# Kernel optimization log

Hardware: AMD Instinct MI355X
Metric: run time of the kernel (lower is better)

## Reference

```python
import jax, jax.numpy as jnp
import numpy as np

B, T, D = 2, 2048, 2048
N, K, H = 16, 4, 128  # query heads, kv heads, head dim
G = N // K            # GQA groups
MIN_TS, MAX_TS = 1.0, 10000.0


def rope(x, positions):
    # x: [B, S, heads, H], positions: [B, S] int
    half = H // 2
    fraction = 2.0 * jnp.arange(half, dtype=jnp.float32) / H
    timescale = MIN_TS * (MAX_TS / MIN_TS) ** fraction            # [half]
    sinusoid = positions.astype(jnp.float32)[:, :, None, None] / timescale  # [B,S,1,half]
    sin, cos = jnp.sin(sinusoid), jnp.cos(sinusoid)
    x1, x2 = x[..., :half], x[..., half:]
    return jnp.concatenate([x1 * cos - x2 * sin, x2 * cos + x1 * sin], axis=-1)


def setup_inputs() -> dict:
    key = jax.random.key(0)
    ks = jax.random.split(key, 6)
    pos = jnp.tile(jnp.arange(T, dtype=jnp.int32)[None, :], (B, 1))
    return {
        "Xq": jax.random.normal(ks[0], (B, T, D), jnp.float32),
        "Xkv": jax.random.normal(ks[1], (B, T, D), jnp.float32),
        "q_positions": pos,
        "kv_positions": pos,
        "Wq": jax.random.normal(ks[2], (D, N, H), jnp.float32) * 0.02,
        "Wk": jax.random.normal(ks[3], (D, K, H), jnp.float32) * 0.02,
        "Wv": jax.random.normal(ks[4], (D, K, H), jnp.float32) * 0.02,
        "Wo": jax.random.normal(ks[5], (N, H, D), jnp.float32) * 0.02,
    }


def reference(Xq, Xkv, q_positions, kv_positions, Wq, Wk, Wv, Wo):
    # QKV projections (tensordot over embed dim), fp32
    q = jnp.einsum("btd,dnh->btnh", Xq, Wq)          # [B,T,N,H]
    k = jnp.einsum("bsd,dkh->bskh", Xkv, Wk)         # [B,S,K,H]
    v = jnp.einsum("bsd,dkh->bskh", Xkv, Wv)
    # inline RoPE on q and k
    q = rope(q, q_positions)
    k = rope(k, kv_positions)
    # GQA: group query heads over kv heads -> [B,K,G,T,H]
    qg = q.transpose(0, 2, 1, 3).reshape(B, K, G, T, H)
    kt = k.transpose(0, 2, 1, 3)                      # [B,K,S,H]
    vt = v.transpose(0, 2, 1, 3)
    scale = 1.0 / jnp.sqrt(jnp.float32(H))
    scores = jnp.einsum("bkgth,bksh->bkgts", qg, kt) * scale
    # causal mask (self-attn, no explicit mask, T>1)
    causal = jnp.tril(jnp.ones((T, T), dtype=bool))
    scores = jnp.where(causal[None, None, None], scores, jnp.finfo(scores.dtype).min)
    probs = jax.nn.softmax(scores, axis=-1)
    attn = jnp.einsum("bkgts,bksh->bkgth", probs, vt)  # [B,K,G,T,H]
    attn = attn.reshape(B, N, T, H).transpose(0, 2, 1, 3)  # [B,T,N,H]
    out = jnp.einsum("btnh,nhd->btd", attn, Wo)
    return out
```

## Files before the change

### kernel.cpp

```cpp
#include <hip/hip_runtime.h>
#include <hip/hip_bf16.h>
#include <cstdint>
#include <cstddef>

#define Bdim 2
#define Tdim 2048
#define Ddim 2048
#define NHq  16
#define NKV  4
#define HD   128
#define SCALE 0.08838834764831845f
#define QPRESCALE (0.08838834764831845f * 1.4426950408889634f)
#define NEG_INF (-3.0e38f)
#define DEFER_THR 11.5f

typedef unsigned short u16;
typedef unsigned int   u32;
typedef __bf16 bf16x8 __attribute__((ext_vector_type(8)));
typedef float  f32x4  __attribute__((ext_vector_type(4)));

__device__ __forceinline__ u16 f2bf(float f) {
    unsigned int u = __float_as_uint(f);
    u += 0x7FFFu + ((u >> 16) & 1u);
    return (u16)(u >> 16);
}
__device__ __forceinline__ u16 f2bfn(float f) {
    __bf16 h = (__bf16)f;
    return __builtin_bit_cast(u16, h);
}
__device__ __forceinline__ float bf2f(u16 s) {
    return __uint_as_float(((unsigned int)s) << 16);
}

#if __has_builtin(__builtin_amdgcn_permlane16_swap) && __has_builtin(__builtin_amdgcn_permlane32_swap)
#define HAVE_PERMLANE_SWAP 1
#endif

__device__ __forceinline__ float quad_reduce_max(float v) {
#ifdef HAVE_PERMLANE_SWAP
    auto r = __builtin_amdgcn_permlane16_swap(__float_as_uint(v), __float_as_uint(v), false, false);
    float m = fmaxf(__uint_as_float(r[0]), __uint_as_float(r[1]));
    auto r2 = __builtin_amdgcn_permlane32_swap(__float_as_uint(m), __float_as_uint(m), false, false);
    return fmaxf(__uint_as_float(r2[0]), __uint_as_float(r2[1]));
#else
    v = fmaxf(v, __shfl_xor(v, 16));
    return fmaxf(v, __shfl_xor(v, 32));
#endif
}
__device__ __forceinline__ float quad_reduce_sum(float v) {
#ifdef HAVE_PERMLANE_SWAP
    auto r = __builtin_amdgcn_permlane16_swap(__float_as_uint(v), __float_as_uint(v), false, false);
    float s = __uint_as_float(r[0]) + __uint_as_float(r[1]);
    auto r2 = __builtin_amdgcn_permlane32_swap(__float_as_uint(s), __float_as_uint(s), false, false);
    return __uint_as_float(r2[0]) + __uint_as_float(r2[1]);
#else
    v += __shfl_xor(v, 16);
    return v + __shfl_xor(v, 32);
#endif
}

__device__ __forceinline__ float tree_max16(const float (&s)[16]) {
    float a0 = fmaxf(s[0], s[1]),  a1 = fmaxf(s[2], s[3]);
    float a2 = fmaxf(s[4], s[5]),  a3 = fmaxf(s[6], s[7]);
    float a4 = fmaxf(s[8], s[9]),  a5 = fmaxf(s[10], s[11]);
    float a6 = fmaxf(s[12], s[13]), a7 = fmaxf(s[14], s[15]);
    float b0 = fmaxf(a0, a1), b1 = fmaxf(a2, a3);
    float b2 = fmaxf(a4, a5), b3 = fmaxf(a6, a7);
    return fmaxf(fmaxf(b0, b1), fmaxf(b2, b3));
}
__device__ __forceinline__ float tree_sum16(const float (&s)[16]) {
    float a0 = s[0] + s[1],  a1 = s[2] + s[3];
    float a2 = s[4] + s[5],  a3 = s[6] + s[7];
    float a4 = s[8] + s[9],  a5 = s[10] + s[11];
    float a6 = s[12] + s[13], a7 = s[14] + s[15];
    float b0 = a0 + a1, b1 = a2 + a3, b2 = a4 + a5, b3 = a6 + a7;
    return (b0 + b1) + (b2 + b3);
}

typedef __attribute__((address_space(1))) const u32 gbl_u32;
typedef __attribute__((address_space(3))) u32 lds_u32;
__device__ __forceinline__ void gload16(const void* g, void* l) {
    __builtin_amdgcn_global_load_lds((gbl_u32*)(uintptr_t)g, (lds_u32*)(uintptr_t)l, 16, 0, 0);
}

#define VM8 asm volatile("s_waitcnt vmcnt(8)" ::: "memory")
#define VM4 asm volatile("s_waitcnt vmcnt(4)" ::: "memory")
#define VM0 asm volatile("s_waitcnt vmcnt(0)" ::: "memory")
#define VMNONE ((void)0)
#define BARRIER do { asm volatile("" ::: "memory"); __builtin_amdgcn_s_barrier(); asm volatile("" ::: "memory"); } while (0)

__global__ __launch_bounds__(256) void prep_all(const float* __restrict__ Xq,
                                                const float* __restrict__ Xkv,
                                                const float* __restrict__ Wq,
                                                const float* __restrict__ Wk,
                                                const float* __restrict__ Wv,
                                                const float* __restrict__ Wo,
                                                u16* __restrict__ xq_bf,
                                                u16* __restrict__ xkv_bf,
                                                u16* __restrict__ wq_t,
                                                u16* __restrict__ wk_t,
                                                u16* __restrict__ wv_t,
                                                u16* __restrict__ wo_t)
{
    __shared__ u16 t[64][72];
    const int tid = threadIdx.x;
    int bid = blockIdx.x;

    if (bid < 8192) {
        const size_t NE = (size_t)4096 * 2048 / 8;
        size_t idx = (size_t)bid * 256 + tid;
        const float* src; u16* dst; size_t off;
        if (idx < NE) { src = Xq;  dst = xq_bf;  off = idx * 8; }
        else          { src = Xkv; dst = xkv_bf; off = (idx - NE) * 8; }
        float4 a = *(const float4*)&src[off];
        float4 b = *(const float4*)&src[off + 4];
        ushort4 r0, r1;
        r0.x = f2bf(a.x); r0.y = f2bf(a.y); r0.z = f2bf(a.z); r0.w = f2bf(a.w);
        r1.x = f2bf(b.x); r1.y = f2bf(b.y); r1.z = f2bf(b.z); r1.w = f2bf(b.w);
        *(ushort4*)&dst[off] = r0;
        *(ushort4*)&dst[off + 4] = r1;
        return;
    }
    bid -= 8192;
    const float* src; u16* dst; int C, gx;
    const int R = 2048;
    if (bid < 1024)      { src = Wq; dst = wq_t; C = 2048; gx = 32; }
    else if (bid < 1280) { src = Wk; dst = wk_t; C = 512;  gx = 8;  bid -= 1024; }
    else if (bid < 1536) { src = Wv; dst = wv_t; C = 512;  gx = 8;  bid -= 1280; }
    else                 { src = Wo; dst = wo_t; C = 2048; gx = 32; bid -= 1536; }

    const int r0 = (bid / gx) * 64, c0 = (bid % gx) * 64;
    const int tr = tid >> 4, tc4 = (tid & 15) * 4;
#pragma unroll
    for (int p = 0; p < 4; p++) {
        int r = p * 16 + tr;
        float4 v = *(const float4*)&src[(size_t)(r0 + r) * C + c0 + tc4];
        t[tc4 + 0][r] = f2bf(v.x);
        t[tc4 + 1][r] = f2bf(v.y);
        t[tc4 + 2][r] = f2bf(v.z);
        t[tc4 + 3][r] = f2bf(v.w);
    }
    __syncthreads();
#pragma unroll
    for (int p = 0; p < 4; p++) {
        int cc = p * 16 + tr;
        ushort4 w = *(const ushort4*)&t[cc][tc4];
        *(ushort4*)&dst[(size_t)(c0 + cc) * R + r0 + tc4] = w;
    }
}

__global__ __launch_bounds__(256) void rope_k(u16* __restrict__ k,
                                              const int* __restrict__ kvpos)
{
    int idx = blockIdx.x * 256 + threadIdx.x;
    int rn = idx >> 4;
    int h4 = (idx & 15) * 4;
    int pos = kvpos[rn >> 2];
    u16* base = k + (size_t)rn * HD;
    ushort4 a = *(const ushort4*)&base[h4];
    ushort4 bvec = *(const ushort4*)&base[h4 + 64];
    u16 av[4] = {a.x, a.y, a.z, a.w};
    u16 bv[4] = {bvec.x, bvec.y, bvec.z, bvec.w};
#pragma unroll
    for (int j = 0; j < 4; j++) {
        float inv_ts = expf(-(float)(h4 + j) * 0.14391156831f);
        float ang = (float)pos * inv_ts;
        float s, c;
        sincosf(ang, &s, &c);
        float x1 = bf2f(av[j]), x2 = bf2f(bv[j]);
        av[j] = f2bf(x1 * c - x2 * s);
        bv[j] = f2bf(x2 * c + x1 * s);
    }
    ushort4 ra, rb;
    ra.x = av[0]; ra.y = av[1]; ra.z = av[2]; ra.w = av[3];
    rb.x = bv[0]; rb.y = bv[1]; rb.z = bv[2]; rb.w = bv[3];
    *(ushort4*)&base[h4] = ra;
    *(ushort4*)&base[h4 + 64] = rb;
}

#define GPH(c, ks, mh, STAGE, VMW) do {                                        \
    bf16x8 Af[4];                                                              \
    _Pragma("unroll")                                                          \
    for (int mf = 0; mf < 4; mf++)                                             \
        Af[mf] = *(const bf16x8*)&Ab[c][ks][(arow + (mh) * 64 + mf * 16) * 32 + cxs]; \
    if ((mh) == 0) {                                                           \
        _Pragma("unroll")                                                      \
        for (int nf = 0; nf < 4; nf++)                                         \
            Bf[nf] = *(const bf16x8*)&Bb[c][ks][(brow + nf * 16) * 32 + cxs];  \
    }                                                                          \
    STAGE;                                                                     \
    BARRIER;                                                                   \
    asm volatile("s_waitcnt lgkmcnt(0)" ::: "memory");                         \
    __builtin_amdgcn_s_setprio(1);                                             \
    _Pragma("unroll")                                                          \
    for (int mf = 0; mf < 4; mf++)                                             \
        _Pragma("unroll")                                                      \
        for (int nf = 0; nf < 4; nf++)                                         \
            acc[(mh) * 4 + mf][nf] = __builtin_amdgcn_mfma_f32_16x16x32_bf16(  \
                Af[mf], Bf[nf], acc[(mh) * 4 + mf][nf], 0, 0, 0);              \
    __builtin_amdgcn_s_setprio(0);                                             \
    VMW;                                                                       \
    BARRIER;                                                                   \
} while (0)

__device__ __forceinline__ void gemm8_mainloop(const u16* __restrict__ A,
                                               const u16* __restrict__ Bt,
                                               int m0, int n0,
                                               u16 (&Ab)[2][2][256 * 32],
                                               u16 (&Bb)[2][2][256 * 32],
                                               f32x4 (&acc)[8][4])
{
    const int tid = threadIdx.x;
    const int wv = tid >> 6, lane = tid & 63;
    const int l15 = lane & 15, quad = lane >> 4;
    const int wr = wv >> 2, wc = wv & 3;

#pragma unroll
    for (int mf = 0; mf < 8; mf++)
#pragma unroll
        for (int nf = 0; nf < 4; nf++) acc[mf][nf] = (f32x4){0.f, 0.f, 0.f, 0.f};

    auto stageA = [&](int kt, int kh, int c) {
#pragma unroll
        for (int j = 0; j < 2; j++) {
            int q = j * 512 + tid;
            int r = q >> 2;
            int c4 = (q & 3) ^ (r & 3);
            gload16(A + (size_t)(m0 + r) * 2048 + kt * 64 + kh * 32 + c4 * 8,
                    &Ab[c][kh][q * 8]);
        }
    };
    auto stageB = [&](int kt, int kh, int c) {
#pragma unroll
        for (int j = 0; j < 2; j++) {
            int q = j * 512 + tid;
            int r = q >> 2;
            int c4 = (q & 3) ^ (r & 3);
            gload16(Bt + (size_t)(n0 + r) * 2048 + kt * 64 + kh * 32 + c4 * 8,
                    &Bb[c][kh][q * 8]);
        }
    };

    const int arow = wr * 128 + l15;
    const int brow = wc * 64 + l15;
    const int cxs  = (quad ^ (l15 & 3)) * 8;

    stageA(0, 0, 0); stageB(0, 0, 0);
    stageA(0, 1, 0); stageB(0, 1, 0);
    stageA(1, 0, 1); stageB(1, 0, 1);
    VM8;
    BARRIER;

    bf16x8 Bf[4];
    for (int it = 0; it < 15; it++) {
        const int t0 = 2 * it, t1 = 2 * it + 1;
        GPH(0, 0, 0, { stageA(t1, 1, 1); },     VMNONE);
        GPH(0, 0, 1, { stageB(t1, 1, 1); },     VM8);
        GPH(0, 1, 0, { stageA(t0 + 2, 0, 0); }, VMNONE);
        GPH(0, 1, 1, { stageB(t0 + 2, 0, 0); }, VM8);
        GPH(1, 0, 0, { stageA(t0 + 2, 1, 0); }, VMNONE);
        GPH(1, 0, 1, { stageB(t0 + 2, 1, 0); }, VM8);
        GPH(1, 1, 0, { stageA(t1 + 2, 0, 1); }, VMNONE);
        GPH(1, 1, 1, { stageB(t1 + 2, 0, 1); }, VM8);
    }
    GPH(0, 0, 0, { stageA(31, 1, 1); }, VMNONE);
    GPH(0, 0, 1, { stageB(31, 1, 1); }, VM8);
    GPH(0, 1, 0, VMNONE, VMNONE);
    GPH(0, 1, 1, VMNONE, VM4);
    GPH(1, 0, 0, VMNONE, VMNONE);
    GPH(1, 0, 1, VMNONE, VM0);
    GPH(1, 1, 0, VMNONE, VMNONE);
    GPH(1, 1, 1, VMNONE, VMNONE);
}

__global__ __launch_bounds__(512, 2) void qkv_gemm8(const u16* __restrict__ Xq,
                                                    const u16* __restrict__ Xkv,
                                                    const u16* __restrict__ Wqt,
                                                    const u16* __restrict__ Wkt,
                                                    const u16* __restrict__ Wvt,
                                                    u16* __restrict__ qraw,
                                                    u16* __restrict__ kraw,
                                                    u16* __restrict__ vt)
{
    __shared__ __align__(16) u16 Ab[2][2][256 * 32];
    __shared__ __align__(16) u16 Bb[2][2][256 * 32];
    f32x4 acc[8][4];

    const int bid0 = (int)blockIdx.x + 12 * (int)blockIdx.y;
    const int swz  = (bid0 & 7) * 24 + (bid0 >> 3);
    const int cx   = swz % 12;
    const int m0   = (swz / 12) * 256;

    const u16 *A, *Bt; int nb;
    if (cx < 8)       { A = Xq;  Bt = Wqt; nb = cx * 256; }
    else if (cx < 10) { A = Xkv; Bt = Wkt; nb = (cx - 8) * 256; }
    else              { A = Xkv; Bt = Wvt; nb = (cx - 10) * 256; }

    gemm8_mainloop(A, Bt, m0, nb, Ab, Bb, acc);

    const int tid = threadIdx.x;
    const int wv = tid >> 6, lane = tid & 63;
    const int l15 = lane & 15, quad = lane >> 4;
    const int wr = wv >> 2, wc = wv & 3;
    const int row0 = m0 + wr * 128;

    if (cx < 10) {
        u16* out; int ldw;
        if (cx < 8) { out = qraw; ldw = 2048; }
        else        { out = kraw; ldw = 512; }
#pragma unroll
        for (int mf = 0; mf < 8; mf++)
#pragma unroll
            for (int nf = 0; nf < 4; nf++) {
                int col = nb + wc * 64 + nf * 16 + l15;
                int r = row0 + mf * 16 + quad * 4;
#pragma unroll
                for (int reg = 0; reg < 4; reg++)
                    out[(size_t)(r + reg) * ldw + col] = f2bf(acc[mf][nf][reg]);
            }
    } else {
        const int b = m0 >> 11;
#pragma unroll
        for (int mf = 0; mf < 8; mf++)
#pragma unroll
            for (int nf = 0; nf < 4; nf++) {
                int col = nb + wc * 64 + nf * 16 + l15;
                int tloc = ((row0 & 2047) + mf * 16 + quad * 4);
                ushort4 w4;
                w4.x = f2bf(acc[mf][nf][0]);
                w4.y = f2bf(acc[mf][nf][1]);
                w4.z = f2bf(acc[mf][nf][2]);
                w4.w = f2bf(acc[mf][nf][3]);
                *(ushort4*)&vt[((size_t)(b * 512 + col)) * 2048 + tloc] = w4;
            }
    }
}

__global__ __launch_bounds__(512, 2) void oproj_gemm8(const u16* __restrict__ attnb,
                                                      const u16* __restrict__ Wot,
                                                      float* __restrict__ out)
{
    __shared__ __align__(16) u16 Ab[2][2][256 * 32];
    __shared__ __align__(16) u16 Bb[2][2][256 * 32];
    f32x4 acc[8][4];

    const int bid0 = (int)blockIdx.x + 8 * (int)blockIdx.y;
    const int swz  = (bid0 & 7) * 16 + (bid0 >> 3);
    const int n0   = (swz % 8) * 256;
    const int m0   = (swz / 8) * 256;

    gemm8_mainloop(attnb, Wot, m0, n0, Ab, Bb, acc);

    const int tid = threadIdx.x;
    const int wv = tid >> 6, lane = tid & 63;
    const int l15 = lane & 15, quad = lane >> 4;
    const int wr = wv >> 2, wc = wv & 3;
    const int row0 = m0 + wr * 128;
#pragma unroll
    for (int mf = 0; mf < 8; mf++)
#pragma unroll
        for (int nf = 0; nf < 4; nf++) {
            int col = n0 + wc * 64 + nf * 16 + l15;
            int r = row0 + mf * 16 + quad * 4;
#pragma unroll
            for (int reg = 0; reg < 4; reg++)
                out[(size_t)(r + reg) * 2048 + col] = acc[mf][nf][reg];
        }
}

__global__ __launch_bounds__(512, 4) void flash_attn_v6(const u16* __restrict__ qh,
                                                        const u16* __restrict__ kh,
                                                        const u16* __restrict__ vtg,
                                                        const int* __restrict__ qpos,
                                                        u16* __restrict__ attnb)
{
    __shared__ __align__(16) u16 Ks[2][64 * 128];
    __shared__ __align__(16) u16 Vt[2][128 * 64];
    __shared__ __align__(16) u16 Ps[128 * 64];

    const int yy = blockIdx.y;
    const int qt = (yy < 8) ? (15 - yy) : (yy - 8);
    const int bh = blockIdx.x;
    const int b = bh >> 4, n = bh & 15, kvh = n >> 2;
    const int q0 = qt * 128;
    const int tid = threadIdx.x;
    const int wv = tid >> 6, lane = tid & 63;
    const int l15 = lane & 15, quad = lane >> 4;

    const size_t kbase = (size_t)(b * Tdim) * 512 + kvh * 128;
    const size_t vbase = ((size_t)(b * 512 + kvh * 128)) * 2048;
    const int nT = 2 * qt + 2;

    auto stage = [&](int t, int buf) {
        const int s0s = t * 64;
#pragma unroll
        for (int c = 0; c < 2; c++) {
            int j = c * 512 + tid;
            int s = j >> 4;
            int c8 = (j & 15) ^ (s & 7);
            gload16(kh + kbase + (size_t)(s0s + s) * 512 + c8 * 8,
                    &Ks[buf][(c * 512 + wv * 64) * 8]);
            int h = j >> 3;
            int sb = (j & 7) ^ (h & 7);
            gload16(vtg + vbase + (size_t)h * 2048 + s0s + sb * 8,
                    &Vt[buf][(c * 512 + wv * 64) * 8]);
        }
    };

    stage(0, 0);

    bf16x8 qfrag[4];
    {
        const size_t qbase = ((size_t)(b * Tdim + q0 + wv * 16)) * 2048 + n * 128;
        float qv[4][8];
#pragma unroll
        for (int kt = 0; kt < 4; kt++) {
            bf16x8 raw = *(const bf16x8*)(qh + qbase + (size_t)l15 * 2048
                                           + kt * 32 + quad * 8);
#pragma unroll
            for (int j = 0; j < 8; j++) qv[kt][j] = (float)raw[j];
        }
        const int pos = qpos[b * Tdim + q0 + wv * 16 + l15];
#pragma unroll
        for (int kt = 0; kt < 2; kt++)
#pragma unroll
            for (int j = 0; j < 8; j++) {
                int h = kt * 32 + quad * 8 + j;
                float inv_ts = expf(-(float)h * 0.14391156831f);
                float s, c;
                sincosf((float)pos * inv_ts, &s, &c);
                s *= QPRESCALE; c *= QPRESCALE;
                float x1 = qv[kt][j], x2 = qv[kt + 2][j];
                qv[kt][j]     = x1 * c - x2 * s;
                qv[kt + 2][j] = x2 * c + x1 * s;
            }
#pragma unroll
        for (int kt = 0; kt < 4; kt++) {
            bf16x8 f;
#pragma unroll
            for (int j = 0; j < 8; j++) f[j] = (__bf16)qv[kt][j];
            qfrag[kt] = f;
        }
    }

    f32x4 Oacc[8];
#pragma unroll
    for (int ht = 0; ht < 8; ht++) Oacc[ht] = (f32x4){0.f, 0.f, 0.f, 0.f};
    float mrow = NEG_INF;
    float lrow = 0.f;

    __syncthreads();

    int cur = 0;
    for (int t = 0; t < nT; t++) {
        const int s0 = t * 64;

        if (t + 1 < nT) stage(t + 1, cur ^ 1);

        f32x4 S[4];
#pragma unroll
        for (int nt = 0; nt < 4; nt++) S[nt] = (f32x4){0.f, 0.f, 0.f, 0.f};
#pragma unroll
        for (int kt = 0; kt < 4; kt++) {
            bf16x8 kf[4];
#pragma unroll
            for (int nt = 0; nt < 4; nt++) {
                int s = nt * 16 + l15;
                int cb = (kt * 4 + quad) ^ (s & 7);
                kf[nt] = *(const bf16x8*)&Ks[cur][s * 128 + cb * 8];
            }
#pragma unroll
            for (int nt = 0; nt < 4; nt++)
                S[nt] = __builtin_amdgcn_mfma_f32_16x16x32_bf16(kf[nt], qfrag[kt], S[nt], 0, 0, 0);
        }

        const bool domask = (t >= nT - 2);
        const int m_l = wv * 16 + l15;
        const int mg = q0 + m_l;
        float sv[16];
#pragma unroll
        for (int nt = 0; nt < 4; nt++)
#pragma unroll
            for (int r = 0; r < 4; r++) {
                float vv = S[nt][r];
                if (domask) {
                    int sg = s0 + nt * 16 + quad * 4 + r;
                    if (sg > mg) vv = NEG_INF;
                }
                sv[nt * 4 + r] = vv;
            }
        float mx = quad_reduce_max(tree_max16(sv));
        const bool skip = __all(mx <= mrow + DEFER_THR);
        const float mNew = skip ? mrow : fmaxf(mrow, mx);
#pragma unroll
        for (int i = 0; i < 16; i++)
            sv[i] = __builtin_amdgcn_exp2f(sv[i] - mNew);
#pragma unroll
        for (int nt = 0; nt < 4; nt++) {
            int sb = nt * 2 + (quad >> 1);
            int cb = sb ^ (m_l & 7);
            ushort4 pw;
            pw.x = f2bfn(sv[nt * 4 + 0]);
            pw.y = f2bfn(sv[nt * 4 + 1]);
            pw.z = f2bfn(sv[nt * 4 + 2]);
            pw.w = f2bfn(sv[nt * 4 + 3]);
            *(ushort4*)&Ps[m_l * 64 + cb * 8 + (quad & 1) * 4] = pw;
        }
        {
            float ps = quad_reduce_sum(tree_sum16(sv));
            if (skip) {
                lrow += ps;
            } else {
                float alpha = __builtin_amdgcn_exp2f(mrow - mNew);
                mrow = mNew;
                lrow = lrow * alpha + ps;
                float a0 = __shfl(alpha, quad * 4 + 0);
                float a1 = __shfl(alpha, quad * 4 + 1);
                float a2 = __shfl(alpha, quad * 4 + 2);
                float a3 = __shfl(alpha, quad * 4 + 3);
#pragma unroll
                for (int ht = 0; ht < 8; ht++) {
                    Oacc[ht][0] *= a0;
                    Oacc[ht][1] *= a1;
                    Oacc[ht][2] *= a2;
                    Oacc[ht][3] *= a3;
                }
            }
        }

#pragma unroll
        for (int k2 = 0; k2 < 2; k2++) {
            int cbp = (k2 * 4 + quad) ^ (m_l & 7);
            bf16x8 pf = *(const bf16x8*)&Ps[m_l * 64 + cbp * 8];
#pragma unroll
            for (int ht = 0; ht < 8; ht++) {
                int h = ht * 16 + l15;
                int cb = (k2 * 4 + quad) ^ (h & 7);
                bf16x8 vf = *(const bf16x8*)&Vt[cur][h * 64 + cb * 8];
                Oacc[ht] = __builtin_amdgcn_mfma_f32_16x16x32_bf16(pf, vf, Oacc[ht], 0, 0, 0);
            }
        }

        __syncthreads();
        cur ^= 1;
    }

    {
        f32x4 inv;
#pragma unroll
        for (int r = 0; r < 4; r++)
            inv[r] = 1.0f / __shfl(lrow, quad * 4 + r);
        int mg0 = q0 + wv * 16 + quad * 4;
        u16* dst0 = attnb + ((size_t)(b * Tdim + mg0)) * 2048 + n * 128 + l15;
#pragma unroll
        for (int ht = 0; ht < 8; ht++) {
#pragma unroll
            for (int r = 0; r < 4; r++)
                dst0[(size_t)r * 2048 + ht * 16] = f2bfn(Oacc[ht][r] * inv[r]);
        }
    }
}

extern "C" void kernel_launch(void* const* d_in, const int* in_sizes, int n_in,
                              void* d_out, int out_size, void* d_ws, size_t ws_size,
                              hipStream_t stream) {
    const float* Xq    = (const float*)d_in[0];
    const float* Xkv   = (const float*)d_in[1];
    const int*   qpos  = (const int*)d_in[2];
    const int*   kvpos = (const int*)d_in[3];
    const float* Wq    = (const float*)d_in[4];
    const float* Wk    = (const float*)d_in[5];
    const float* Wv    = (const float*)d_in[6];
    const float* Wo    = (const float*)d_in[7];
    float* out = (float*)d_out;

    char* w = (char*)d_ws;
    u16* xq_bf = (u16*)(w);
    u16* xkv_bf= (u16*)(w + (16u << 20));
    u16* qraw  = (u16*)(w + (32u << 20));
    u16* kraw  = (u16*)(w + (48u << 20));
    u16* vt    = (u16*)(w + (52u << 20));
    u16* wq_t  = (u16*)(w + (56u << 20));
    u16* wk_t  = (u16*)(w + (64u << 20));
    u16* wv_t  = (u16*)(w + (66u << 20));
    u16* wo_t  = (u16*)(w + (68u << 20));
    u16* attnb = (u16*)(w);

    prep_all<<<10752, 256, 0, stream>>>(Xq, Xkv, Wq, Wk, Wv, Wo,
                                        xq_bf, xkv_bf, wq_t, wk_t, wv_t, wo_t);
    qkv_gemm8<<<dim3(12, 16), 512, 0, stream>>>(xq_bf, xkv_bf, wq_t, wk_t, wv_t,
                                                qraw, kraw, vt);
    rope_k<<<1024, 256, 0, stream>>>(kraw, kvpos);
    flash_attn_v6<<<dim3(32, 16), 512, 0, stream>>>(qraw, kraw, vt, qpos, attnb);
    oproj_gemm8<<<dim3(8, 16), 512, 0, stream>>>(attnb, wo_t, out);
}
```

Baseline: 349.0 us.

## Narrow o-proj GEMM tiles to 256x128 and use hardware sincos for RoPE

```diff
diff --git a/kernel.cpp b/kernel.cpp
--- a/kernel.cpp
+++ b/kernel.cpp
@@ -13,6 +13,8 @@
 #define QPRESCALE (0.08838834764831845f * 1.4426950408889634f)
 #define NEG_INF (-3.0e38f)
 #define DEFER_THR 11.5f
+#define ROPE_L2 0.20762051f
+#define INV_2PI 0.15915494f
 
 typedef unsigned short u16;
 typedef unsigned int   u32;
@@ -30,6 +32,12 @@
 }
 __device__ __forceinline__ float bf2f(u16 s) {
     return __uint_as_float(((unsigned int)s) << 16);
+}
+
+__device__ __forceinline__ void hw_sincos_rev(float rev, float* s, float* c) {
+    rev -= floorf(rev);
+    *s = __builtin_amdgcn_sinf(rev);
+    *c = __builtin_amdgcn_cosf(rev);
 }
 
 #if __has_builtin(__builtin_amdgcn_permlane16_swap) && __has_builtin(__builtin_amdgcn_permlane32_swap)
@@ -84,7 +92,9 @@
 }
 
 #define VM8 asm volatile("s_waitcnt vmcnt(8)" ::: "memory")
+#define VM6 asm volatile("s_waitcnt vmcnt(6)" ::: "memory")
 #define VM4 asm volatile("s_waitcnt vmcnt(4)" ::: "memory")
+#define VM3 asm volatile("s_waitcnt vmcnt(3)" ::: "memory")
 #define VM0 asm volatile("s_waitcnt vmcnt(0)" ::: "memory")
 #define VMNONE ((void)0)
 #define BARRIER do { asm volatile("" ::: "memory"); __builtin_amdgcn_s_barrier(); asm volatile("" ::: "memory"); } while (0)
@@ -163,10 +173,9 @@
     u16 bv[4] = {bvec.x, bvec.y, bvec.z, bvec.w};
 #pragma unroll
     for (int j = 0; j < 4; j++) {
-        float inv_ts = expf(-(float)(h4 + j) * 0.14391156831f);
-        float ang = (float)pos * inv_ts;
+        float rscale = __builtin_amdgcn_exp2f((float)(h4 + j) * -ROPE_L2) * INV_2PI;
         float s, c;
-        sincosf(ang, &s, &c);
+        hw_sincos_rev((float)pos * rscale, &s, &c);
         float x1 = bf2f(av[j]), x2 = bf2f(bv[j]);
         av[j] = f2bf(x1 * c - x2 * s);
         bv[j] = f2bf(x2 * c + x1 * s);
@@ -336,20 +345,112 @@
     }
 }
 
-__global__ __launch_bounds__(512, 2) void oproj_gemm8(const u16* __restrict__ attnb,
-                                                      const u16* __restrict__ Wot,
-                                                      float* __restrict__ out)
+#define GPHN(c, ks, mh, STAGE, VMW) do {                                       \
+    bf16x8 Af[4];                                                              \
+    _Pragma("unroll")                                                          \
+    for (int mf = 0; mf < 4; mf++)                                             \
+        Af[mf] = *(const bf16x8*)&Ab[c][ks][(arow + (mh) * 64 + mf * 16) * 32 + cxs]; \
+    if ((mh) == 0) {                                                           \
+        _Pragma("unroll")                                                      \
+        for (int nf = 0; nf < 2; nf++)                                         \
+            Bf[nf] = *(const bf16x8*)&Bb[c][ks][(brow + nf * 16) * 32 + cxs];  \
+    }                                                                          \
+    STAGE;                                                                     \
+    BARRIER;                                                                   \
+    asm volatile("s_waitcnt lgkmcnt(0)" ::: "memory");                         \
+    __builtin_amdgcn_s_setprio(1);                                             \
+    _Pragma("unroll")                                                          \
+    for (int mf = 0; mf < 4; mf++)                                             \
+        _Pragma("unroll")                                                      \
+        for (int nf = 0; nf < 2; nf++)                                         \
+            acc[(mh) * 4 + mf][nf] = __builtin_amdgcn_mfma_f32_16x16x32_bf16(  \
+                Af[mf], Bf[nf], acc[(mh) * 4 + mf][nf], 0, 0, 0);              \
+    __builtin_amdgcn_s_setprio(0);                                             \
+    VMW;                                                                       \
+    BARRIER;                                                                   \
+} while (0)
+
+__device__ __forceinline__ void gemm8n_mainloop(const u16* __restrict__ A,
+                                                const u16* __restrict__ Bt,
+                                                int m0, int n0,
+                                                u16 (&Ab)[2][2][256 * 32],
+                                                u16 (&Bb)[2][2][128 * 32],
+                                                f32x4 (&acc)[8][2])
+{
+    const int tid = threadIdx.x;
+    const int wv = tid >> 6, lane = tid & 63;
+    const int l15 = lane & 15, quad = lane >> 4;
+    const int wr = wv >> 2, wc = wv & 3;
+
+#pragma unroll
+    for (int mf = 0; mf < 8; mf++)
+#pragma unroll
+        for (int nf = 0; nf < 2; nf++) acc[mf][nf] = (f32x4){0.f, 0.f, 0.f, 0.f};
+
+    auto stageA = [&](int kt, int kh, int c) {
+#pragma unroll
+        for (int j = 0; j < 2; j++) {
+            int q = j * 512 + tid;
+            int r = q >> 2;
+            int c4 = (q & 3) ^ (r & 3);
+            gload16(A + (size_t)(m0 + r) * 2048 + kt * 64 + kh * 32 + c4 * 8,
+                    &Ab[c][kh][q * 8]);
+        }
+    };
+    auto stageB = [&](int kt, int kh, int c) {
+        int q = tid;
+        int r = q >> 2;
+        int c4 = (q & 3) ^ (r & 3);
+        gload16(Bt + (size_t)(n0 + r) * 2048 + kt * 64 + kh * 32 + c4 * 8,
+                &Bb[c][kh][q * 8]);
+    };
+
+    const int arow = wr * 128 + l15;
+    const int brow = wc * 32 + l15;
+    const int cxs  = (quad ^ (l15 & 3)) * 8;
+
+    stageA(0, 0, 0); stageB(0, 0, 0);
+    stageA(0, 1, 0); stageB(0, 1, 0);
+    stageA(1, 0, 1); stageB(1, 0, 1);
+    VM6;
+    BARRIER;
+
+    bf16x8 Bf[2];
+    for (int it = 0; it < 15; it++) {
+        const int t0 = 2 * it, t1 = 2 * it + 1;
+        GPHN(0, 0, 0, { stageA(t1, 1, 1); },     VMNONE);
+        GPHN(0, 0, 1, { stageB(t1, 1, 1); },     VM6);
+        GPHN(0, 1, 0, { stageA(t0 + 2, 0, 0); }, VMNONE);
+        GPHN(0, 1, 1, { stageB(t0 + 2, 0, 0); }, VM6);
+        GPHN(1, 0, 0, { stageA(t0 + 2, 1, 0); }, VMNONE);
+        GPHN(1, 0, 1, { stageB(t0 + 2, 1, 0); }, VM6);
+        GPHN(1, 1, 0, { stageA(t1 + 2, 0, 1); }, VMNONE);
+        GPHN(1, 1, 1, { stageB(t1 + 2, 0, 1); }, VM6);
+    }
+    GPHN(0, 0, 0, { stageA(31, 1, 1); }, VMNONE);
+    GPHN(0, 0, 1, { stageB(31, 1, 1); }, VM6);
+    GPHN(0, 1, 0, VMNONE, VMNONE);
+    GPHN(0, 1, 1, VMNONE, VM3);
+    GPHN(1, 0, 0, VMNONE, VMNONE);
+    GPHN(1, 0, 1, VMNONE, VM0);
+    GPHN(1, 1, 0, VMNONE, VMNONE);
+    GPHN(1, 1, 1, VMNONE, VMNONE);
+}
+
+__global__ __launch_bounds__(512, 2) void oproj_gemm8n(const u16* __restrict__ attnb,
+                                                       const u16* __restrict__ Wot,
+                                                       float* __restrict__ out)
 {
     __shared__ __align__(16) u16 Ab[2][2][256 * 32];
-    __shared__ __align__(16) u16 Bb[2][2][256 * 32];
-    f32x4 acc[8][4];
-
-    const int bid0 = (int)blockIdx.x + 8 * (int)blockIdx.y;
-    const int swz  = (bid0 & 7) * 16 + (bid0 >> 3);
-    const int n0   = (swz % 8) * 256;
-    const int m0   = (swz / 8) * 256;
-
-    gemm8_mainloop(attnb, Wot, m0, n0, Ab, Bb, acc);
+    __shared__ __align__(16) u16 Bb[2][2][128 * 32];
+    f32x4 acc[8][2];
+
+    const int bid0 = (int)blockIdx.x + 16 * (int)blockIdx.y;
+    const int swz  = (bid0 & 7) * 32 + (bid0 >> 3);
+    const int n0   = (swz % 16) * 128;
+    const int m0   = (swz / 16) * 256;
+
+    gemm8n_mainloop(attnb, Wot, m0, n0, Ab, Bb, acc);
 
     const int tid = threadIdx.x;
     const int wv = tid >> 6, lane = tid & 63;
@@ -359,8 +460,8 @@
 #pragma unroll
     for (int mf = 0; mf < 8; mf++)
 #pragma unroll
-        for (int nf = 0; nf < 4; nf++) {
-            int col = n0 + wc * 64 + nf * 16 + l15;
+        for (int nf = 0; nf < 2; nf++) {
+            int col = n0 + wc * 32 + nf * 16 + l15;
             int r = row0 + mf * 16 + quad * 4;
 #pragma unroll
             for (int reg = 0; reg < 4; reg++)
@@ -368,7 +469,7 @@
         }
 }
 
-__global__ __launch_bounds__(512, 4) void flash_attn_v6(const u16* __restrict__ qh,
+__global__ __launch_bounds__(512, 4) void flash_attn_v7(const u16* __restrict__ qh,
                                                         const u16* __restrict__ kh,
                                                         const u16* __restrict__ vtg,
                                                         const int* __restrict__ qpos,
@@ -412,35 +513,24 @@
     bf16x8 qfrag[4];
     {
         const size_t qbase = ((size_t)(b * Tdim + q0 + wv * 16)) * 2048 + n * 128;
-        float qv[4][8];
-#pragma unroll
-        for (int kt = 0; kt < 4; kt++) {
-            bf16x8 raw = *(const bf16x8*)(qh + qbase + (size_t)l15 * 2048
-                                           + kt * 32 + quad * 8);
-#pragma unroll
-            for (int j = 0; j < 8; j++) qv[kt][j] = (float)raw[j];
-        }
-        const int pos = qpos[b * Tdim + q0 + wv * 16 + l15];
+#pragma unroll
+        for (int kt = 0; kt < 4; kt++)
+            qfrag[kt] = *(const bf16x8*)(qh + qbase + (size_t)l15 * 2048
+                                          + kt * 32 + quad * 8);
+        const float fpos = (float)qpos[b * Tdim + q0 + wv * 16 + l15];
 #pragma unroll
         for (int kt = 0; kt < 2; kt++)
 #pragma unroll
             for (int j = 0; j < 8; j++) {
                 int h = kt * 32 + quad * 8 + j;
-                float inv_ts = expf(-(float)h * 0.14391156831f);
+                float rscale = __builtin_amdgcn_exp2f((float)h * -ROPE_L2) * INV_2PI;
                 float s, c;
-                sincosf((float)pos * inv_ts, &s, &c);
+                hw_sincos_rev(fpos * rscale, &s, &c);
                 s *= QPRESCALE; c *= QPRESCALE;
-                float x1 = qv[kt][j], x2 = qv[kt + 2][j];
-                qv[kt][j]     = x1 * c - x2 * s;
-                qv[kt + 2][j] = x2 * c + x1 * s;
+                float x1 = (float)qfrag[kt][j], x2 = (float)qfrag[kt + 2][j];
+                qfrag[kt][j]     = (__bf16)(x1 * c - x2 * s);
+                qfrag[kt + 2][j] = (__bf16)(x2 * c + x1 * s);
             }
-#pragma unroll
-        for (int kt = 0; kt < 4; kt++) {
-            bf16x8 f;
-#pragma unroll
-            for (int j = 0; j < 8; j++) f[j] = (__bf16)qv[kt][j];
-            qfrag[kt] = f;
-        }
     }
 
     f32x4 Oacc[8];
@@ -591,6 +681,6 @@
     qkv_gemm8<<<dim3(12, 16), 512, 0, stream>>>(xq_bf, xkv_bf, wq_t, wk_t, wv_t,
                                                 qraw, kraw, vt);
     rope_k<<<1024, 256, 0, stream>>>(kraw, kvpos);
-    flash_attn_v6<<<dim3(32, 16), 512, 0, stream>>>(qraw, kraw, vt, qpos, attnb);
-    oproj_gemm8<<<dim3(8, 16), 512, 0, stream>>>(attnb, wo_t, out);
-}
+    flash_attn_v7<<<dim3(32, 16), 512, 0, stream>>>(qraw, kraw, vt, qpos, attnb);
+    oproj_gemm8n<<<dim3(16, 16), 512, 0, stream>>>(attnb, wo_t, out);
+}
```

New measurement: 308.8 us. 1.13x faster.
